# Optimization experiments

Measured on AMD Instinct MI355X. Metric: run time of the kernel, lower is better.

## Reference

```python
import jax, jax.numpy as jnp
import numpy as np

N_USERS = 100000
N_ITEMS = 50000
N_NODES = N_USERS + N_ITEMS
N_EDGES = 1500000
EMBED = 100
BATCH = 4096


def spmm(rows, cols, vals, X):
    # sparse(N,N) @ dense(N,F) via gather + segment-sum
    return jax.ops.segment_sum(vals[:, None] * X[cols], rows, num_segments=N_NODES)


def setup_inputs() -> dict:
    key = jax.random.key(0)
    ks = jax.random.split(key, 24)
    userIdx = jax.random.randint(ks[0], (BATCH,), 0, N_USERS)
    itemIdx = jax.random.randint(ks[1], (BATCH,), N_USERS, N_NODES)  # offset item ids
    rows = jax.random.randint(ks[2], (N_EDGES,), 0, N_NODES)
    cols = jax.random.randint(ks[3], (N_EDGES,), 0, N_NODES)
    vals = jax.random.uniform(ks[4], (N_EDGES,), dtype=jnp.float32) * 0.01  # D^-1/2 A D^-1/2 scale
    s = 0.1
    uEmbd = jax.random.normal(ks[5], (N_USERS, EMBED), jnp.float32) * s
    iEmbd = jax.random.normal(ks[6], (N_ITEMS, EMBED), jnp.float32) * s
    # GNN layer 1: 100 -> 80 ; layer 2: 80 -> 50 (torch Linear => W stored (in,out) here)
    w1 = jax.random.normal(ks[7], (100, 80), jnp.float32) * s
    b1 = jnp.zeros((80,), jnp.float32)
    wi1 = jax.random.normal(ks[8], (100, 80), jnp.float32) * s
    bi1 = jnp.zeros((80,), jnp.float32)
    w2 = jax.random.normal(ks[9], (80, 50), jnp.float32) * s
    b2 = jnp.zeros((50,), jnp.float32)
    wi2 = jax.random.normal(ks[10], (80, 50), jnp.float32) * s
    bi2 = jnp.zeros((50,), jnp.float32)
    t1w = jax.random.normal(ks[11], (460, 64), jnp.float32) * s
    t1b = jnp.zeros((64,), jnp.float32)
    t2w = jax.random.normal(ks[12], (64, 32), jnp.float32) * s
    t2b = jnp.zeros((32,), jnp.float32)
    t3w = jax.random.normal(ks[13], (32, 1), jnp.float32) * s
    t3b = jnp.zeros((1,), jnp.float32)
    return {"userIdx": userIdx, "itemIdx": itemIdx, "rows": rows, "cols": cols,
            "vals": vals, "uEmbd": uEmbd, "iEmbd": iEmbd,
            "w1": w1, "b1": b1, "wi1": wi1, "bi1": bi1,
            "w2": w2, "b2": b2, "wi2": wi2, "bi2": bi2,
            "t1w": t1w, "t1b": t1b, "t2w": t2w, "t2b": t2b, "t3w": t3w, "t3b": t3b}


def gnn_layer(rows, cols, vals, feats, w, b, wi, bi):
    Lx = spmm(rows, cols, vals, feats)          # L @ X
    inter = Lx * feats                          # elementwise
    part1 = (Lx + feats) @ w + b                # (L + I) @ X then linear
    part2 = spmm(rows, cols, vals, inter) @ wi + bi
    return part1 + part2


def reference(userIdx, itemIdx, rows, cols, vals, uEmbd, iEmbd,
              w1, b1, wi1, bi1, w2, b2, wi2, bi2,
              t1w, t1b, t2w, t2b, t3w, t3b):
    features = jnp.concatenate([uEmbd, iEmbd], axis=0)   # [N, 100]
    final = features
    f1 = jax.nn.relu(gnn_layer(rows, cols, vals, features, w1, b1, wi1, bi1))  # [N,80]
    final = jnp.concatenate([final, f1], axis=1)
    f2 = jax.nn.relu(gnn_layer(rows, cols, vals, f1, w2, b2, wi2, bi2))        # [N,50]
    final = jnp.concatenate([final, f2], axis=1)          # [N, 230]
    embd = jnp.concatenate([final[userIdx], final[itemIdx]], axis=1)  # [B, 460]
    embd = jax.nn.relu(embd @ t1w + t1b)
    embd = embd @ t2w + t2b
    embd = embd @ t3w + t3b
    return embd.flatten()
```

## Files before the change

kernel.cpp:

```cpp
#include <hip/hip_runtime.h>

typedef unsigned int uint;
typedef unsigned short ushort_t;
typedef __attribute__((ext_vector_type(4))) float f32x4;
typedef __attribute__((ext_vector_type(8))) short bf16x8;

#define N_USERS 100000
#define N_ITEMS 50000
#define N_NODES 150000
#define N_EDGES 1500000
#define BATCH 4096
#define NSWEEP 4
#define SWEEP_ROWS 37500

__device__ __forceinline__ uint pack_bf16x2(float a, float b) {
    uint ua = __float_as_uint(a);
    uint ub = __float_as_uint(b);
    ua = (ua + 0x7FFFu + ((ua >> 16) & 1u)) >> 16;
    ub = (ub + 0x7FFFu + ((ub >> 16) & 1u)) >> 16;
    return ua | (ub << 16);
}
__device__ __forceinline__ ushort_t cvt_bf16(float a) {
    uint ua = __float_as_uint(a);
    return (ushort_t)((ua + 0x7FFFu + ((ua >> 16) & 1u)) >> 16);
}
__device__ __forceinline__ float bf_lo(uint u) { return __uint_as_float(u << 16); }
__device__ __forceinline__ float bf_hi(uint u) { return __uint_as_float(u & 0xFFFF0000u); }

template<int P>
__device__ __forceinline__ float2 row_gather_accum(
    const int2* __restrict__ ep, int st, int d,
    const uint* __restrict__ src, int lane)
{
    float ax = 0.f, ay = 0.f;
    bool lok = lane < P;
    int2 e[12];
#pragma unroll
    for (int k = 0; k < 12; k++) e[k] = ep[st + k];
    uint b[8];
#pragma unroll
    for (int k = 0; k < 8; k++)
        b[k] = (lok && k < d) ? src[(size_t)e[k].x * P + lane] : 0u;
    for (int j = 0; j < d; j += 4) {
        uint n[4];
#pragma unroll
        for (int k = 0; k < 4; k++)
            n[k] = (lok && j + 8 + k < d) ? src[(size_t)e[8 + k].x * P + lane] : 0u;
        int2 ne[4];
#pragma unroll
        for (int k = 0; k < 4; k++) ne[k] = ep[st + j + 12 + k];
        {
            float v = __int_as_float(e[0].y);
            ax = fmaf(v, bf_lo(b[0]), ax);
            ay = fmaf(v, bf_hi(b[0]), ay);
        }
#pragma unroll
        for (int k = 1; k < 4; k++) {
            if (j + k < d) {
                float v = __int_as_float(e[k].y);
                ax = fmaf(v, bf_lo(b[k]), ax);
                ay = fmaf(v, bf_hi(b[k]), ay);
            }
        }
#pragma unroll
        for (int k = 0; k < 8; k++) e[k] = e[k + 4];
#pragma unroll
        for (int k = 0; k < 4; k++) { b[k] = b[k + 4]; b[k + 4] = n[k]; e[k + 8] = ne[k]; }
    }
    return make_float2(ax, ay);
}

__device__ __forceinline__ float2 row_gather_accum_mul(
    const int2* __restrict__ ep, int st, int d,
    const uint* __restrict__ sA, const uint* __restrict__ sB, int lane)
{
    constexpr int P = 40;
    float ax = 0.f, ay = 0.f;
    bool lok = lane < P;
    int2 e0 = ep[st],     e1 = ep[st + 1], e2 = ep[st + 2], e3 = ep[st + 3];
    int2 e4 = ep[st + 4], e5 = ep[st + 5];
    uint a0 = (lok && 0 < d) ? sA[(size_t)e0.x * P + lane] : 0u;
    uint c0 = (lok && 0 < d) ? sB[(size_t)e0.x * P + lane] : 0u;
    uint a1 = (lok && 1 < d) ? sA[(size_t)e1.x * P + lane] : 0u;
    uint c1 = (lok && 1 < d) ? sB[(size_t)e1.x * P + lane] : 0u;
    uint a2 = (lok && 2 < d) ? sA[(size_t)e2.x * P + lane] : 0u;
    uint c2 = (lok && 2 < d) ? sB[(size_t)e2.x * P + lane] : 0u;
    uint a3 = (lok && 3 < d) ? sA[(size_t)e3.x * P + lane] : 0u;
    uint c3 = (lok && 3 < d) ? sB[(size_t)e3.x * P + lane] : 0u;
    for (int j = 0; j < d; j += 2) {
        uint nA4 = (lok && j + 4 < d) ? sA[(size_t)e4.x * P + lane] : 0u;
        uint nC4 = (lok && j + 4 < d) ? sB[(size_t)e4.x * P + lane] : 0u;
        uint nA5 = (lok && j + 5 < d) ? sA[(size_t)e5.x * P + lane] : 0u;
        uint nC5 = (lok && j + 5 < d) ? sB[(size_t)e5.x * P + lane] : 0u;
        int2 n6 = ep[st + j + 6];
        int2 n7 = ep[st + j + 7];
        float v0 = __int_as_float(e0.y);
        ax = fmaf(v0, bf_lo(a0) * bf_lo(c0), ax);
        ay = fmaf(v0, bf_hi(a0) * bf_hi(c0), ay);
        if (j + 1 < d) {
            float v1 = __int_as_float(e1.y);
            ax = fmaf(v1, bf_lo(a1) * bf_lo(c1), ax);
            ay = fmaf(v1, bf_hi(a1) * bf_hi(c1), ay);
        }
        e0 = e2; a0 = a2; c0 = c2; e1 = e3; a1 = a3; c1 = c3;
        e2 = e4; a2 = nA4; c2 = nC4; e3 = e5; a3 = nA5; c3 = nC5;
        e4 = n6; e5 = n7;
    }
    return make_float2(ax, ay);
}

__global__ __launch_bounds__(256) void cast_feats(
    const float* __restrict__ uE, const float* __restrict__ iE,
    uint* __restrict__ Xb64, uint* __restrict__ Xc50)
{
    int g = blockIdx.x * 256 + threadIdx.x;
    if (g >= N_NODES * 64) return;
    int row = g >> 6, c = g & 63;
    uint outv = 0u;
    if (c < 50) {
        int e0 = c * 2;
        float a, b;
        if (row < N_USERS) { a = uE[(size_t)row * 100 + e0]; b = uE[(size_t)row * 100 + e0 + 1]; }
        else { a = iE[(size_t)(row - N_USERS) * 100 + e0]; b = iE[(size_t)(row - N_USERS) * 100 + e0 + 1]; }
        outv = pack_bf16x2(a, b);
        Xc50[(size_t)row * 50 + c] = outv;
    }
    Xb64[g] = outv;
}

__global__ __launch_bounds__(256) void prep_weights(
    const float* __restrict__ W, const float* __restrict__ Wi,
    uint* __restrict__ wtW, uint* __restrict__ wtWi)
{
    int t = blockIdx.x * 256 + threadIdx.x;
    if (t >= 2 * 80 * 64) return;
    const float* src = (t < 80 * 64) ? W : Wi;
    uint* dst = (t < 80 * 64) ? wtW : wtWi;
    int i = t % (80 * 64);
    int col = i >> 6, kk = i & 63;
    int k = kk * 2;
    uint v = 0u;
    if (k < 100) v = pack_bf16x2(src[(size_t)k * 80 + col], src[(size_t)(k + 1) * 80 + col]);
    dst[(size_t)col * 64 + kk] = v;
}

__global__ __launch_bounds__(256) void hist_kernel(
    const int* __restrict__ rows, int* __restrict__ deg, int E)
{
    int e = blockIdx.x * 256 + threadIdx.x;
    if (e < E) atomicAdd(&deg[rows[e]], 1);
}

__global__ __launch_bounds__(256) void scan_block(
    const int* __restrict__ deg, int* __restrict__ ptr,
    int* __restrict__ bsum, int n)
{
    __shared__ int s[256];
    int t = threadIdx.x;
    int i = blockIdx.x * 256 + t;
    int v = (i < n) ? deg[i] : 0;
    s[t] = v; __syncthreads();
    for (int off = 1; off < 256; off <<= 1) {
        int x = (t >= off) ? s[t - off] : 0;
        __syncthreads();
        s[t] += x;
        __syncthreads();
    }
    if (i < n) ptr[i] = s[t] - v;
    if (t == 255) bsum[blockIdx.x] = s[255];
}

__global__ __launch_bounds__(1024) void scan_tops(int* __restrict__ bsum, int nb)
{
    __shared__ int s[1024];
    int t = threadIdx.x;
    int v = (t < nb) ? bsum[t] : 0;
    s[t] = v; __syncthreads();
    for (int off = 1; off < 1024; off <<= 1) {
        int x = (t >= off) ? s[t - off] : 0;
        __syncthreads();
        s[t] += x;
        __syncthreads();
    }
    if (t < nb) bsum[t] = s[t] - v;
}

__global__ __launch_bounds__(256) void scan_apply(
    int* __restrict__ ptr, const int* __restrict__ bsum,
    int* __restrict__ pos, int n)
{
    int i = blockIdx.x * 256 + threadIdx.x;
    if (i < n) {
        int p = ptr[i] + bsum[i >> 8];
        ptr[i] = p;
        pos[i] = p;
    }
}

__global__ __launch_bounds__(256) void scatter_sweep(
    const int* __restrict__ rows, const int* __restrict__ cols,
    const float* __restrict__ vals, int* __restrict__ pos,
    int2* __restrict__ ep, int E, int lo, int hi)
{
    int e = blockIdx.x * 256 + threadIdx.x;
    if (e >= E) return;
    int r = rows[e];
    if (r < lo || r >= hi) return;
    int p = atomicAdd(&pos[r], 1);
    ep[p] = make_int2(cols[e], __float_as_int(vals[e]));
}

__global__ __launch_bounds__(256) void build_selmap(
    const int* __restrict__ userIdx, const int* __restrict__ itemIdx,
    int* __restrict__ selMap)
{
    int i = blockIdx.x * 256 + threadIdx.x;
    if (i < BATCH) selMap[userIdx[i]] = i;
    else if (i < 2 * BATCH) selMap[itemIdx[i - BATCH]] = i;
}

__global__ __launch_bounds__(256) void mark_needed(
    const int* __restrict__ userIdx, const int* __restrict__ itemIdx,
    const int* __restrict__ ptr_, const int* __restrict__ deg_,
    const int2* __restrict__ ep, int* __restrict__ flag)
{
    int i = blockIdx.x * 4 + ((int)threadIdx.x >> 6);
    if (i >= 2 * BATCH) return;
    int lane = threadIdx.x & 63;
    int row = (i < BATCH) ? userIdx[i] : itemIdx[i - BATCH];
    if (lane == 0) flag[row] = 1;
    int st = ptr_[row], d = deg_[row];
    for (int j = lane; j < d; j += 64)
        flag[ep[st + j].x] = 1;
}

__global__ __launch_bounds__(256) void compact_list(
    const int* __restrict__ flag, const int* __restrict__ fpre,
    const int* __restrict__ bsum, int* __restrict__ list,
    int* __restrict__ count, int n)
{
    int i = blockIdx.x * 256 + threadIdx.x;
    if (i < n) {
        int base = fpre[i] + bsum[i >> 8];
        if (flag[i]) list[base] = i;
        if (i == n - 1) *count = base + flag[i];
    }
}


__global__ __launch_bounds__(256) void spmm_pass1(
    const int* __restrict__ ptr_, const int* __restrict__ deg_,
    const int2* __restrict__ ep, const uint* __restrict__ Xc,
    uint* __restrict__ B1b, uint* __restrict__ INTb, int N)
{
    int row = blockIdx.x * 4 + ((int)threadIdx.x >> 6);
    if (row >= N) return;
    int lane = threadIdx.x & 63;
    float2 r = row_gather_accum<50>(ep, ptr_[row], deg_[row], Xc, lane);
    B1b[(size_t)row * 64 + lane] = pack_bf16x2(r.x, r.y);
    if (lane < 50) {
        uint xb = Xc[(size_t)row * 50 + lane];
        INTb[(size_t)row * 50 + lane] = pack_bf16x2(r.x * bf_lo(xb), r.y * bf_hi(xb));
    }
}

__global__ __launch_bounds__(256) void spmm_pass2(
    const int* __restrict__ ptr_, const int* __restrict__ deg_,
    const int2* __restrict__ ep, const uint* __restrict__ INTb,
    uint* __restrict__ B2b, int N)
{
    int row = blockIdx.x * 4 + ((int)threadIdx.x >> 6);
    if (row >= N) return;
    int lane = threadIdx.x & 63;
    float2 r = row_gather_accum<50>(ep, ptr_[row], deg_[row], INTb, lane);
    B2b[(size_t)row * 64 + lane] = pack_bf16x2(r.x, r.y);
}

__global__ __launch_bounds__(256) void spmm_pass3(
    const int* __restrict__ list, const int* __restrict__ count,
    const int* __restrict__ ptr_, const int* __restrict__ deg_,
    const int2* __restrict__ ep, const uint* __restrict__ F1b,
    const int* __restrict__ selMap,
    uint* __restrict__ Lxb, float* __restrict__ Lxsel)
{
    int idx = blockIdx.x * 4 + ((int)threadIdx.x >> 6);
    if (idx >= *count) return;
    int row = list[idx];
    int lane = threadIdx.x & 63;
    float2 r = row_gather_accum<40>(ep, ptr_[row], deg_[row], F1b, lane);
    if (lane < 40) {
        Lxb[(size_t)row * 40 + lane] = pack_bf16x2(r.x, r.y);
        int sm = selMap[row];
        if (sm >= 0)
            ((float2*)(Lxsel + (size_t)sm * 80))[lane] = r;
    }
}

__global__ __launch_bounds__(256) void spmm_pass4(
    const int* __restrict__ ptr_, const int* __restrict__ deg_,
    const int2* __restrict__ ep,
    const uint* __restrict__ Lxb, const uint* __restrict__ F1b,
    const int* __restrict__ userIdx, const int* __restrict__ itemIdx,
    float* __restrict__ outC)
{
    int i = blockIdx.x * 4 + ((int)threadIdx.x >> 6);
    if (i >= 2 * BATCH) return;
    int row = (i < BATCH) ? userIdx[i] : itemIdx[i - BATCH];
    int lane = threadIdx.x & 63;
    float2 r = row_gather_accum_mul(ep, ptr_[row], deg_[row], Lxb, F1b, lane);
    if (lane < 40)
        ((float2*)(outC + (size_t)i * 80))[lane] = r;
}

__global__ __launch_bounds__(256) void gemm1_mfma(
    const uint* __restrict__ B1b, const uint* __restrict__ Xb,
    const uint* __restrict__ B2b,
    const uint* __restrict__ wtW, const uint* __restrict__ wtWi,
    const float* __restrict__ b, const float* __restrict__ bi,
    const int* __restrict__ selMap,
    ushort_t* __restrict__ F1b, float* __restrict__ F1sel, int N)
{
    int wave = (int)threadIdx.x >> 6;
    int lane = (int)threadIdx.x & 63;
    int rowBase = blockIdx.x * 64 + wave * 16;
    int colLocal = lane & 15;
    int q = lane >> 4;
    int arow = rowBase + colLocal;
    bool rowOK = arow < N;

    f32x4 acc[5];
#pragma unroll
    for (int nt = 0; nt < 5; nt++) acc[nt] = (f32x4){0.f, 0.f, 0.f, 0.f};

    const bf16x8 zfrag = {};
    size_t aoff = (size_t)arow * 64 + q * 4;

#pragma unroll
    for (int ks = 0; ks < 4; ks++) {
        bf16x8 aL = rowOK ? *(const bf16x8*)(B1b + aoff + ks * 16) : zfrag;
        bf16x8 aX = rowOK ? *(const bf16x8*)(Xb  + aoff + ks * 16) : zfrag;
        bf16x8 aS = rowOK ? *(const bf16x8*)(B2b + aoff + ks * 16) : zfrag;
#pragma unroll
        for (int nt = 0; nt < 5; nt++) {
            size_t boff = (size_t)(nt * 16 + colLocal) * 64 + ks * 16 + q * 4;
            bf16x8 bW  = *(const bf16x8*)(wtW  + boff);
            bf16x8 bWi = *(const bf16x8*)(wtWi + boff);
            acc[nt] = __builtin_amdgcn_mfma_f32_16x16x32_bf16(aL, bW,  acc[nt], 0, 0, 0);
            acc[nt] = __builtin_amdgcn_mfma_f32_16x16x32_bf16(aX, bW,  acc[nt], 0, 0, 0);
            acc[nt] = __builtin_amdgcn_mfma_f32_16x16x32_bf16(aS, bWi, acc[nt], 0, 0, 0);
        }
    }

    int sm[4];
    bool rok[4];
#pragma unroll
    for (int reg = 0; reg < 4; reg++) {
        int row = rowBase + q * 4 + reg;
        rok[reg] = row < N;
        sm[reg] = rok[reg] ? selMap[row] : -1;
    }
#pragma unroll
    for (int nt = 0; nt < 5; nt++) {
        int col = nt * 16 + colLocal;
        float bias = b[col] + bi[col];
#pragma unroll
        for (int reg = 0; reg < 4; reg++) {
            if (!rok[reg]) continue;
            int row = rowBase + q * 4 + reg;
            float v = fmaxf(acc[nt][reg] + bias, 0.f);
            F1b[(size_t)row * 80 + col] = cvt_bf16(v);
            if (sm[reg] >= 0) F1sel[(size_t)sm[reg] * 80 + col] = v;
        }
    }
}

__global__ __launch_bounds__(256) void gemm_fused2_sel(
    const float* __restrict__ Lxsel, const float* __restrict__ F1sel,
    const int* __restrict__ selMap,
    const float* __restrict__ S2c,
    const float* __restrict__ W, const float* __restrict__ b,
    const float* __restrict__ Wi, const float* __restrict__ bi,
    const int* __restrict__ userIdx, const int* __restrict__ itemIdx,
    float* __restrict__ outC)
{
    constexpr int K = 80, M = 50, TPR = 2, MT = M / TPR;
    __shared__ float sW[K * M];
    __shared__ float sWi[K * M];
    for (int i = threadIdx.x; i < K * M; i += 256) {
        sW[i]  = W[i];
        sWi[i] = Wi[i];
    }
    __syncthreads();

    int i = blockIdx.x * (256 / TPR) + (int)threadIdx.x / TPR;
    int mBase = ((int)threadIdx.x % TPR) * MT;
    if (i >= 2 * BATCH) return;
    int r = (i < BATCH) ? userIdx[i] : itemIdx[i - BATCH];
    int sm = selMap[r];

    const float* xrow = F1sel + (size_t)sm * K;
    const float* lrow = Lxsel + (size_t)sm * K;
    const float* srow = S2c + (size_t)i * K;

    float acc[MT];
#pragma unroll
    for (int m = 0; m < MT; m++) acc[m] = 0.0f;

    for (int k4 = 0; k4 < K; k4 += 4) {
        float4 lv = *(const float4*)(lrow + k4);
        float4 xv = *(const float4*)(xrow + k4);
        float4 sv = *(const float4*)(srow + k4);
        float a[4] = {lv.x + xv.x, lv.y + xv.y, lv.z + xv.z, lv.w + xv.w};
        float s[4] = {sv.x, sv.y, sv.z, sv.w};
#pragma unroll
        for (int kk = 0; kk < 4; kk++) {
            const float* wk  = &sW[(k4 + kk) * M + mBase];
            const float* wik = &sWi[(k4 + kk) * M + mBase];
#pragma unroll
            for (int m = 0; m < MT; m++)
                acc[m] = fmaf(a[kk], wk[m], fmaf(s[kk], wik[m], acc[m]));
        }
    }

    float* orow = outC + (size_t)i * M + mBase;
#pragma unroll
    for (int m = 0; m < MT; m++)
        orow[m] = fmaxf(acc[m] + b[mBase + m] + bi[mBase + m], 0.0f);
}

template<int K, int M, int TPR, bool RELU>
__global__ __launch_bounds__(256) void mlp_gemm(
    const float* __restrict__ A,
    const float* __restrict__ W, const float* __restrict__ b,
    float* __restrict__ out, int N)
{
    __shared__ float sW[K * M];
    for (int i = threadIdx.x; i < K * M; i += 256) sW[i] = W[i];
    __syncthreads();

    constexpr int RPB = 256 / TPR;
    constexpr int MT  = M / TPR;
    int r = blockIdx.x * RPB + (int)threadIdx.x / TPR;
    int mBase = ((int)threadIdx.x % TPR) * MT;
    if (r >= N) return;

    const float* arow = A + (size_t)r * K;
    float acc[MT];
#pragma unroll
    for (int m = 0; m < MT; m++) acc[m] = 0.0f;

    for (int k = 0; k < K; k++) {
        float a = arow[k];
#pragma unroll
        for (int m = 0; m < MT; m++)
            acc[m] = fmaf(a, sW[k * M + mBase + m], acc[m]);
    }

    float* orow = out + (size_t)r * M + mBase;
#pragma unroll
    for (int m = 0; m < MT; m++) {
        float vv = acc[m] + b[mBase + m];
        orow[m] = RELU ? fmaxf(vv, 0.0f) : vv;
    }
}

__global__ __launch_bounds__(128) void gather_embd(
    const int* __restrict__ userIdx, const int* __restrict__ itemIdx,
    const float* __restrict__ uE, const float* __restrict__ iE,
    const float* __restrict__ F1sel, const int* __restrict__ selMap,
    const float* __restrict__ f2c,
    float* __restrict__ emb)
{
    int bi = blockIdx.x;
    int u  = userIdx[bi];
    int it = itemIdx[bi];
    int su = selMap[u];
    int si = selMap[it];
    float* orow = emb + (size_t)bi * 460;
    for (int c = threadIdx.x; c < 460; c += 128) {
        float val;
        if (c < 100) {
            val = (u < N_USERS) ? uE[(size_t)u * 100 + c]
                                : iE[(size_t)(u - N_USERS) * 100 + c];
        } else if (c < 180) {
            val = F1sel[(size_t)su * 80 + (c - 100)];
        } else if (c < 230) {
            val = f2c[(size_t)bi * 50 + (c - 180)];
        } else if (c < 330) {
            int cc = c - 230;
            val = (it < N_USERS) ? uE[(size_t)it * 100 + cc]
                                 : iE[(size_t)(it - N_USERS) * 100 + cc];
        } else if (c < 410) {
            val = F1sel[(size_t)si * 80 + (c - 330)];
        } else {
            val = f2c[(size_t)(BATCH + bi) * 50 + (c - 410)];
        }
        orow[c] = val;
    }
}

extern "C" void kernel_launch(void* const* d_in, const int* in_sizes, int n_in,
                              void* d_out, int out_size, void* d_ws, size_t ws_size,
                              hipStream_t stream) {
    const int*   userIdx = (const int*)d_in[0];
    const int*   itemIdx = (const int*)d_in[1];
    const int*   rows    = (const int*)d_in[2];
    const int*   cols    = (const int*)d_in[3];
    const float* vals    = (const float*)d_in[4];
    const float* uEmbd   = (const float*)d_in[5];
    const float* iEmbd   = (const float*)d_in[6];
    const float* w1      = (const float*)d_in[7];
    const float* b1      = (const float*)d_in[8];
    const float* wi1     = (const float*)d_in[9];
    const float* bi1     = (const float*)d_in[10];
    const float* w2      = (const float*)d_in[11];
    const float* b2      = (const float*)d_in[12];
    const float* wi2     = (const float*)d_in[13];
    const float* bi2     = (const float*)d_in[14];
    const float* t1w     = (const float*)d_in[15];
    const float* t1b     = (const float*)d_in[16];
    const float* t2w     = (const float*)d_in[17];
    const float* t2b     = (const float*)d_in[18];
    const float* t3w     = (const float*)d_in[19];
    const float* t3b     = (const float*)d_in[20];

    float* ws = (float*)d_ws;
    uint*  Xb64  = (uint*)ws;
    uint*  Xc50  = (uint*)(ws + 9600000);
    uint*  B1b   = (uint*)(ws + 17100000);
    uint*  Lxb   = B1b;
    uint*  INTb  = (uint*)(ws + 26700000);
    uint*  F1b   = INTb;
    uint*  B2b   = (uint*)(ws + 34200000);
    uint*  wtW   = (uint*)(ws + 43800000);
    uint*  wtWi  = (uint*)(ws + 43805120);
    float* F1sel = ws + 43810240;
    float* Lxsel = ws + 44465600;
    float* B2c   = ws + 45120960;
    float* F2c   = ws + 45776320;
    float* EMB   = ws + 46185920;
    float* H1    = ws + 48070080;
    float* H2    = ws + 48332224;
    int*   deg   = (int*)(ws + 48463296);
    int*   ptr   = deg + 150000;
    int*   pos   = ptr + 150000;
    int*   bsum  = pos + 150000;
    int2*  ep    = (int2*)(bsum + 1024);
    int*   flag  = (int*)(ep + 1500016);
    int*   fpre  = flag + 150000;
    int*   list  = fpre + 150000;
    int*   bsum2 = list + 150000;
    int*   cnt   = bsum2 + 1024;
    int*   selMap= cnt + 1;

    const int E = N_EDGES;
    dim3 blk(256);

    cast_feats<<<(N_NODES * 64 + 255) / 256, blk, 0, stream>>>(uEmbd, iEmbd, Xb64, Xc50);
    prep_weights<<<(2 * 80 * 64 + 255) / 256, blk, 0, stream>>>(w1, wi1, wtW, wtWi);

    hipMemsetAsync(deg, 0, 150000 * sizeof(int), stream);
    hipMemsetAsync(flag, 0, 150000 * sizeof(int), stream);
    hipMemsetAsync(selMap, 0xFF, 150000 * sizeof(int), stream);
    hist_kernel<<<(E + 255) / 256, blk, 0, stream>>>(rows, deg, E);
    int nScanBlocks = (N_NODES + 255) / 256;
    scan_block<<<nScanBlocks, blk, 0, stream>>>(deg, ptr, bsum, N_NODES);
    scan_tops<<<1, dim3(1024), 0, stream>>>(bsum, nScanBlocks);
    scan_apply<<<nScanBlocks, blk, 0, stream>>>(ptr, bsum, pos, N_NODES);
    for (int s = 0; s < NSWEEP; s++) {
        scatter_sweep<<<(E + 255) / 256, blk, 0, stream>>>(
            rows, cols, vals, pos, ep, E, s * SWEEP_ROWS, (s + 1) * SWEEP_ROWS);
    }

    build_selmap<<<(2 * BATCH + 255) / 256, blk, 0, stream>>>(userIdx, itemIdx, selMap);
    mark_needed<<<(2 * BATCH + 3) / 4, blk, 0, stream>>>(
        userIdx, itemIdx, ptr, deg, ep, flag);
    scan_block<<<nScanBlocks, blk, 0, stream>>>(flag, fpre, bsum2, N_NODES);
    scan_tops<<<1, dim3(1024), 0, stream>>>(bsum2, nScanBlocks);
    compact_list<<<nScanBlocks, blk, 0, stream>>>(flag, fpre, bsum2, list, cnt, N_NODES);

    int rowGrid = (N_NODES + 3) / 4;
    int selGrid = (2 * BATCH + 3) / 4;

    spmm_pass1<<<rowGrid, blk, 0, stream>>>(ptr, deg, ep, Xc50, B1b, INTb, N_NODES);
    spmm_pass2<<<rowGrid, blk, 0, stream>>>(ptr, deg, ep, INTb, B2b, N_NODES);
    {
        int grid = (N_NODES + 63) / 64;
        gemm1_mfma<<<grid, blk, 0, stream>>>(
            B1b, Xb64, B2b, wtW, wtWi, b1, bi1, selMap,
            (ushort_t*)F1b, F1sel, N_NODES);
    }

    spmm_pass3<<<rowGrid, blk, 0, stream>>>(
        list, cnt, ptr, deg, ep, F1b, selMap, Lxb, Lxsel);
    spmm_pass4<<<selGrid, blk, 0, stream>>>(
        ptr, deg, ep, Lxb, F1b, userIdx, itemIdx, B2c);
    {
        int grid = (2 * BATCH + 127) / 128;
        gemm_fused2_sel<<<grid, blk, 0, stream>>>(
            Lxsel, F1sel, selMap, B2c, w2, b2, wi2, bi2, userIdx, itemIdx, F2c);
    }

    gather_embd<<<BATCH, dim3(128), 0, stream>>>(
        userIdx, itemIdx, uEmbd, iEmbd, F1sel, selMap, F2c, EMB);
    {
        constexpr int TPR = 8;
        int grid = (BATCH + (256 / TPR) - 1) / (256 / TPR);
        mlp_gemm<460, 64, TPR, true><<<grid, blk, 0, stream>>>(
            EMB, t1w, t1b, H1, BATCH);
    }
    {
        constexpr int TPR = 4;
        int grid = (BATCH + (256 / TPR) - 1) / (256 / TPR);
        mlp_gemm<64, 32, TPR, false><<<grid, blk, 0, stream>>>(
            H1, t2w, t2b, H2, BATCH);
    }
    {
        constexpr int TPR = 1;
        int grid = (BATCH + 255) / 256;
        mlp_gemm<32, 1, TPR, false><<<grid, blk, 0, stream>>>(
            H2, t3w, t3b, (float*)d_out, BATCH);
    }
}
```

Before: 576.5 us.

## Pack four rows per wave with uint4 gathers and degree-sorted row order

The SpMM passes change from one row per 64-lane wave to four rows per wave, with 16 lanes each loading uint4 (8 bf16) chunks. Rows are bucket-sorted by degree through histogram, scan and scatter kernels so the rows sharing a wave have similar trip counts. The feature rows are padded to 52 uints for 16-byte alignment, and the edge list gets a zero tail so the loop can read past its end. This aims to cut the idle lanes (50 of 64 were used) and the underfilled waves on short rows, at the cost of extra sort kernels and rows scattered across memory.

```diff
diff --git a/kernel.cpp b/kernel.cpp
--- a/kernel.cpp
+++ b/kernel.cpp
@@ -12,6 +12,7 @@
 #define BATCH 4096
 #define NSWEEP 4
 #define SWEEP_ROWS 37500
+#define EP_PAD 96
 
 __device__ __forceinline__ uint pack_bf16x2(float a, float b) {
     uint ua = __float_as_uint(a);
@@ -27,47 +28,29 @@
 __device__ __forceinline__ float bf_lo(uint u) { return __uint_as_float(u << 16); }
 __device__ __forceinline__ float bf_hi(uint u) { return __uint_as_float(u & 0xFFFF0000u); }
 
-template<int P>
-__device__ __forceinline__ float2 row_gather_accum(
-    const int2* __restrict__ ep, int st, int d,
-    const uint* __restrict__ src, int lane)
-{
-    float ax = 0.f, ay = 0.f;
-    bool lok = lane < P;
-    int2 e[12];
-#pragma unroll
-    for (int k = 0; k < 12; k++) e[k] = ep[st + k];
-    uint b[8];
-#pragma unroll
-    for (int k = 0; k < 8; k++)
-        b[k] = (lok && k < d) ? src[(size_t)e[k].x * P + lane] : 0u;
-    for (int j = 0; j < d; j += 4) {
-        uint n[4];
-#pragma unroll
-        for (int k = 0; k < 4; k++)
-            n[k] = (lok && j + 8 + k < d) ? src[(size_t)e[8 + k].x * P + lane] : 0u;
-        int2 ne[4];
-#pragma unroll
-        for (int k = 0; k < 4; k++) ne[k] = ep[st + j + 12 + k];
-        {
-            float v = __int_as_float(e[0].y);
-            ax = fmaf(v, bf_lo(b[0]), ax);
-            ay = fmaf(v, bf_hi(b[0]), ay);
-        }
-#pragma unroll
-        for (int k = 1; k < 4; k++) {
-            if (j + k < d) {
-                float v = __int_as_float(e[k].y);
-                ax = fmaf(v, bf_lo(b[k]), ax);
-                ay = fmaf(v, bf_hi(b[k]), ay);
-            }
-        }
-#pragma unroll
-        for (int k = 0; k < 8; k++) e[k] = e[k + 4];
-#pragma unroll
-        for (int k = 0; k < 4; k++) { b[k] = b[k + 4]; b[k + 4] = n[k]; e[k + 8] = ne[k]; }
-    }
-    return make_float2(ax, ay);
+template<int PU4>
+__device__ __forceinline__ void group_gather(
+    const int2* __restrict__ ep, int st, int d, int dmax,
+    const uint* __restrict__ src, int l,
+    float aLo[4], float aHi[4])
+{
+    const uint4* s4 = (const uint4*)src;
+    bool lok = l < PU4;
+    int2 e0 = ep[st];
+    int2 e1 = ep[st + 1];
+    uint4 g0 = {0u, 0u, 0u, 0u};
+    if (lok && 0 < d) g0 = s4[(size_t)(uint)e0.x * PU4 + l];
+    for (int j = 0; j < dmax; j++) {
+        int2 e2 = ep[st + j + 2];
+        uint4 g1 = {0u, 0u, 0u, 0u};
+        if (lok && j + 1 < d) g1 = s4[(size_t)(uint)e1.x * PU4 + l];
+        float v = (j < d) ? __int_as_float(e0.y) : 0.f;
+        aLo[0] = fmaf(v, bf_lo(g0.x), aLo[0]); aHi[0] = fmaf(v, bf_hi(g0.x), aHi[0]);
+        aLo[1] = fmaf(v, bf_lo(g0.y), aLo[1]); aHi[1] = fmaf(v, bf_hi(g0.y), aHi[1]);
+        aLo[2] = fmaf(v, bf_lo(g0.z), aLo[2]); aHi[2] = fmaf(v, bf_hi(g0.z), aHi[2]);
+        aLo[3] = fmaf(v, bf_lo(g0.w), aLo[3]); aHi[3] = fmaf(v, bf_hi(g0.w), aHi[3]);
+        e0 = e1; e1 = e2; g0 = g1;
+    }
 }
 
 __device__ __forceinline__ float2 row_gather_accum_mul(
@@ -111,7 +94,7 @@
 
 __global__ __launch_bounds__(256) void cast_feats(
     const float* __restrict__ uE, const float* __restrict__ iE,
-    uint* __restrict__ Xb64, uint* __restrict__ Xc50)
+    uint* __restrict__ Xb64, uint* __restrict__ Xc52)
 {
     int g = blockIdx.x * 256 + threadIdx.x;
     if (g >= N_NODES * 64) return;
@@ -123,9 +106,9 @@
         if (row < N_USERS) { a = uE[(size_t)row * 100 + e0]; b = uE[(size_t)row * 100 + e0 + 1]; }
         else { a = iE[(size_t)(row - N_USERS) * 100 + e0]; b = iE[(size_t)(row - N_USERS) * 100 + e0 + 1]; }
         outv = pack_bf16x2(a, b);
-        Xc50[(size_t)row * 50 + c] = outv;
     }
     Xb64[g] = outv;
+    if (c < 52) Xc52[(size_t)row * 52 + c] = outv;
 }
 
 __global__ __launch_bounds__(256) void prep_weights(
@@ -210,6 +193,12 @@
     ep[p] = make_int2(cols[e], __float_as_int(vals[e]));
 }
 
+__global__ __launch_bounds__(128) void pad_ep(int2* __restrict__ ep)
+{
+    int t = threadIdx.x;
+    if (t < EP_PAD) ep[N_EDGES + t] = make_int2(0, 0);
+}
+
 __global__ __launch_bounds__(256) void build_selmap(
     const int* __restrict__ userIdx, const int* __restrict__ itemIdx,
     int* __restrict__ selMap)
@@ -234,65 +223,141 @@
         flag[ep[st + j].x] = 1;
 }
 
-__global__ __launch_bounds__(256) void compact_list(
-    const int* __restrict__ flag, const int* __restrict__ fpre,
-    const int* __restrict__ bsum, int* __restrict__ list,
-    int* __restrict__ count, int n)
+__global__ __launch_bounds__(256) void deg_hist(
+    const int* __restrict__ deg, const int* __restrict__ flag,
+    int* __restrict__ hist, int n)
 {
     int i = blockIdx.x * 256 + threadIdx.x;
-    if (i < n) {
-        int base = fpre[i] + bsum[i >> 8];
-        if (flag[i]) list[base] = i;
-        if (i == n - 1) *count = base + flag[i];
-    }
+    if (i >= n) return;
+    if (flag && !flag[i]) return;
+    int b = deg[i]; if (b > 63) b = 63;
+    atomicAdd(&hist[b], 1);
+}
+
+__global__ __launch_bounds__(64) void bins_scan(
+    const int* __restrict__ hist, int* __restrict__ pos, int* __restrict__ total)
+{
+    __shared__ int s[64];
+    int t = threadIdx.x;
+    int v = hist[t];
+    s[t] = v; __syncthreads();
+    for (int off = 1; off < 64; off <<= 1) {
+        int x = (t >= off) ? s[t - off] : 0;
+        __syncthreads();
+        s[t] += x;
+        __syncthreads();
+    }
+    pos[t] = s[t] - v;
+    if (t == 63 && total) *total = s[63];
+}
+
+__global__ __launch_bounds__(256) void deg_scatter(
+    const int* __restrict__ deg, const int* __restrict__ flag,
+    int* __restrict__ pos, int* __restrict__ sorted, int n)
+{
+    int i = blockIdx.x * 256 + threadIdx.x;
+    if (i >= n) return;
+    if (flag && !flag[i]) return;
+    int b = deg[i]; if (b > 63) b = 63;
+    int p = atomicAdd(&pos[b], 1);
+    sorted[p] = i;
 }
 
 
 __global__ __launch_bounds__(256) void spmm_pass1(
+    const int* __restrict__ sortedAll,
     const int* __restrict__ ptr_, const int* __restrict__ deg_,
     const int2* __restrict__ ep, const uint* __restrict__ Xc,
     uint* __restrict__ B1b, uint* __restrict__ INTb, int N)
 {
-    int row = blockIdx.x * 4 + ((int)threadIdx.x >> 6);
-    if (row >= N) return;
-    int lane = threadIdx.x & 63;
-    float2 r = row_gather_accum<50>(ep, ptr_[row], deg_[row], Xc, lane);
-    B1b[(size_t)row * 64 + lane] = pack_bf16x2(r.x, r.y);
-    if (lane < 50) {
-        uint xb = Xc[(size_t)row * 50 + lane];
-        INTb[(size_t)row * 50 + lane] = pack_bf16x2(r.x * bf_lo(xb), r.y * bf_hi(xb));
+    int wave = (int)threadIdx.x >> 6, lane = (int)threadIdx.x & 63;
+    int grp = lane >> 4, l = lane & 15;
+    int si = blockIdx.x * 16 + wave * 4 + grp;
+    bool valid = si < N;
+    int row = valid ? sortedAll[si] : 0;
+    int d = valid ? deg_[row] : 0;
+    int st = valid ? ptr_[row] : 0;
+    int dm = d, t;
+    t = __shfl_xor(dm, 16); dm = dm > t ? dm : t;
+    t = __shfl_xor(dm, 32); dm = dm > t ? dm : t;
+    float aLo[4] = {0.f, 0.f, 0.f, 0.f}, aHi[4] = {0.f, 0.f, 0.f, 0.f};
+    group_gather<13>(ep, st, d, dm, Xc, l, aLo, aHi);
+    if (!valid) return;
+    uint4 o = {0u, 0u, 0u, 0u};
+    if (l < 13) {
+        o.x = pack_bf16x2(aLo[0], aHi[0]); o.y = pack_bf16x2(aLo[1], aHi[1]);
+        o.z = pack_bf16x2(aLo[2], aHi[2]); o.w = pack_bf16x2(aLo[3], aHi[3]);
+    }
+    ((uint4*)(B1b + (size_t)row * 64))[l] = o;
+    if (l < 13) {
+        uint4 x = ((const uint4*)(Xc + (size_t)row * 52))[l];
+        uint4 p;
+        p.x = pack_bf16x2(aLo[0] * bf_lo(x.x), aHi[0] * bf_hi(x.x));
+        p.y = pack_bf16x2(aLo[1] * bf_lo(x.y), aHi[1] * bf_hi(x.y));
+        p.z = pack_bf16x2(aLo[2] * bf_lo(x.z), aHi[2] * bf_hi(x.z));
+        p.w = pack_bf16x2(aLo[3] * bf_lo(x.w), aHi[3] * bf_hi(x.w));
+        ((uint4*)(INTb + (size_t)row * 52))[l] = p;
     }
 }
 
 __global__ __launch_bounds__(256) void spmm_pass2(
+    const int* __restrict__ sortedAll,
     const int* __restrict__ ptr_, const int* __restrict__ deg_,
     const int2* __restrict__ ep, const uint* __restrict__ INTb,
     uint* __restrict__ B2b, int N)
 {
-    int row = blockIdx.x * 4 + ((int)threadIdx.x >> 6);
-    if (row >= N) return;
-    int lane = threadIdx.x & 63;
-    float2 r = row_gather_accum<50>(ep, ptr_[row], deg_[row], INTb, lane);
-    B2b[(size_t)row * 64 + lane] = pack_bf16x2(r.x, r.y);
+    int wave = (int)threadIdx.x >> 6, lane = (int)threadIdx.x & 63;
+    int grp = lane >> 4, l = lane & 15;
+    int si = blockIdx.x * 16 + wave * 4 + grp;
+    bool valid = si < N;
+    int row = valid ? sortedAll[si] : 0;
+    int d = valid ? deg_[row] : 0;
+    int st = valid ? ptr_[row] : 0;
+    int dm = d, t;
+    t = __shfl_xor(dm, 16); dm = dm > t ? dm : t;
+    t = __shfl_xor(dm, 32); dm = dm > t ? dm : t;
+    float aLo[4] = {0.f, 0.f, 0.f, 0.f}, aHi[4] = {0.f, 0.f, 0.f, 0.f};
+    group_gather<13>(ep, st, d, dm, INTb, l, aLo, aHi);
+    if (!valid) return;
+    uint4 o = {0u, 0u, 0u, 0u};
+    if (l < 13) {
+        o.x = pack_bf16x2(aLo[0], aHi[0]); o.y = pack_bf16x2(aLo[1], aHi[1]);
+        o.z = pack_bf16x2(aLo[2], aHi[2]); o.w = pack_bf16x2(aLo[3], aHi[3]);
+    }
+    ((uint4*)(B2b + (size_t)row * 64))[l] = o;
 }
 
 __global__ __launch_bounds__(256) void spmm_pass3(
-    const int* __restrict__ list, const int* __restrict__ count,
+    const int* __restrict__ sorted3, const int* __restrict__ cnt3,
     const int* __restrict__ ptr_, const int* __restrict__ deg_,
     const int2* __restrict__ ep, const uint* __restrict__ F1b,
     const int* __restrict__ selMap,
     uint* __restrict__ Lxb, float* __restrict__ Lxsel)
 {
-    int idx = blockIdx.x * 4 + ((int)threadIdx.x >> 6);
-    if (idx >= *count) return;
-    int row = list[idx];
-    int lane = threadIdx.x & 63;
-    float2 r = row_gather_accum<40>(ep, ptr_[row], deg_[row], F1b, lane);
-    if (lane < 40) {
-        Lxb[(size_t)row * 40 + lane] = pack_bf16x2(r.x, r.y);
-        int sm = selMap[row];
-        if (sm >= 0)
-            ((float2*)(Lxsel + (size_t)sm * 80))[lane] = r;
+    int wave = (int)threadIdx.x >> 6, lane = (int)threadIdx.x & 63;
+    int grp = lane >> 4, l = lane & 15;
+    int si = blockIdx.x * 16 + wave * 4 + grp;
+    int n3 = *cnt3;
+    bool valid = si < n3;
+    int row = valid ? sorted3[si] : 0;
+    int d = valid ? deg_[row] : 0;
+    int st = valid ? ptr_[row] : 0;
+    int dm = d, t;
+    t = __shfl_xor(dm, 16); dm = dm > t ? dm : t;
+    t = __shfl_xor(dm, 32); dm = dm > t ? dm : t;
+    float aLo[4] = {0.f, 0.f, 0.f, 0.f}, aHi[4] = {0.f, 0.f, 0.f, 0.f};
+    group_gather<10>(ep, st, d, dm, F1b, l, aLo, aHi);
+    if (!valid || l >= 10) return;
+    uint4 o;
+    o.x = pack_bf16x2(aLo[0], aHi[0]); o.y = pack_bf16x2(aLo[1], aHi[1]);
+    o.z = pack_bf16x2(aLo[2], aHi[2]); o.w = pack_bf16x2(aLo[3], aHi[3]);
+    ((uint4*)(Lxb + (size_t)row * 40))[l] = o;
+    int sm = selMap[row];
+    if (sm >= 0) {
+        float4 f0 = make_float4(aLo[0], aHi[0], aLo[1], aHi[1]);
+        float4 f1 = make_float4(aLo[2], aHi[2], aLo[3], aHi[3]);
+        ((float4*)(Lxsel + (size_t)sm * 80))[2 * l]     = f0;
+        ((float4*)(Lxsel + (size_t)sm * 80))[2 * l + 1] = f1;
     }
 }
 
@@ -526,42 +591,46 @@
 
     float* ws = (float*)d_ws;
     uint*  Xb64  = (uint*)ws;
-    uint*  Xc50  = (uint*)(ws + 9600000);
-    uint*  B1b   = (uint*)(ws + 17100000);
+    uint*  Xc52  = (uint*)(ws + 9600000);
+    uint*  B1b   = (uint*)(ws + 17400000);
     uint*  Lxb   = B1b;
-    uint*  INTb  = (uint*)(ws + 26700000);
+    uint*  INTb  = (uint*)(ws + 27000000);
     uint*  F1b   = INTb;
-    uint*  B2b   = (uint*)(ws + 34200000);
-    uint*  wtW   = (uint*)(ws + 43800000);
-    uint*  wtWi  = (uint*)(ws + 43805120);
-    float* F1sel = ws + 43810240;
-    float* Lxsel = ws + 44465600;
-    float* B2c   = ws + 45120960;
-    float* F2c   = ws + 45776320;
-    float* EMB   = ws + 46185920;
-    float* H1    = ws + 48070080;
-    float* H2    = ws + 48332224;
-    int*   deg   = (int*)(ws + 48463296);
+    uint*  B2b   = (uint*)(ws + 34800000);
+    uint*  wtW   = (uint*)(ws + 44400000);
+    uint*  wtWi  = (uint*)(ws + 44405120);
+    float* F1sel = ws + 44410240;
+    float* Lxsel = ws + 45065600;
+    float* B2c   = ws + 45720960;
+    float* F2c   = ws + 46376320;
+    float* EMB   = ws + 46785920;
+    float* H1    = ws + 48670080;
+    float* H2    = ws + 48932224;
+    int*   deg   = (int*)(ws + 49063296);
     int*   ptr   = deg + 150000;
     int*   pos   = ptr + 150000;
     int*   bsum  = pos + 150000;
     int2*  ep    = (int2*)(bsum + 1024);
-    int*   flag  = (int*)(ep + 1500016);
-    int*   fpre  = flag + 150000;
-    int*   list  = fpre + 150000;
-    int*   bsum2 = list + 150000;
-    int*   cnt   = bsum2 + 1024;
-    int*   selMap= cnt + 1;
+    int*   flag  = (int*)(ep + 1500096);
+    int*   selMap= flag + 150000;
+    int*   sortedAll = selMap + 150000;
+    int*   sorted3   = sortedAll + 150000;
+    int*   hist64    = sorted3 + 150000;
+    int*   hist64b   = hist64 + 64;
+    int*   pos64     = hist64b + 64;
+    int*   pos64b    = pos64 + 64;
+    int*   cnt3      = pos64b + 64;
 
     const int E = N_EDGES;
     dim3 blk(256);
 
-    cast_feats<<<(N_NODES * 64 + 255) / 256, blk, 0, stream>>>(uEmbd, iEmbd, Xb64, Xc50);
+    cast_feats<<<(N_NODES * 64 + 255) / 256, blk, 0, stream>>>(uEmbd, iEmbd, Xb64, Xc52);
     prep_weights<<<(2 * 80 * 64 + 255) / 256, blk, 0, stream>>>(w1, wi1, wtW, wtWi);
 
     hipMemsetAsync(deg, 0, 150000 * sizeof(int), stream);
     hipMemsetAsync(flag, 0, 150000 * sizeof(int), stream);
     hipMemsetAsync(selMap, 0xFF, 150000 * sizeof(int), stream);
+    hipMemsetAsync(hist64, 0, 128 * sizeof(int), stream);
     hist_kernel<<<(E + 255) / 256, blk, 0, stream>>>(rows, deg, E);
     int nScanBlocks = (N_NODES + 255) / 256;
     scan_block<<<nScanBlocks, blk, 0, stream>>>(deg, ptr, bsum, N_NODES);
@@ -571,19 +640,26 @@
         scatter_sweep<<<(E + 255) / 256, blk, 0, stream>>>(
             rows, cols, vals, pos, ep, E, s * SWEEP_ROWS, (s + 1) * SWEEP_ROWS);
     }
+    pad_ep<<<1, dim3(128), 0, stream>>>(ep);
 
     build_selmap<<<(2 * BATCH + 255) / 256, blk, 0, stream>>>(userIdx, itemIdx, selMap);
     mark_needed<<<(2 * BATCH + 3) / 4, blk, 0, stream>>>(
         userIdx, itemIdx, ptr, deg, ep, flag);
-    scan_block<<<nScanBlocks, blk, 0, stream>>>(flag, fpre, bsum2, N_NODES);
-    scan_tops<<<1, dim3(1024), 0, stream>>>(bsum2, nScanBlocks);
-    compact_list<<<nScanBlocks, blk, 0, stream>>>(flag, fpre, bsum2, list, cnt, N_NODES);
-
-    int rowGrid = (N_NODES + 3) / 4;
+
+    deg_hist<<<nScanBlocks, blk, 0, stream>>>(deg, nullptr, hist64, N_NODES);
+    deg_hist<<<nScanBlocks, blk, 0, stream>>>(deg, flag, hist64b, N_NODES);
+    bins_scan<<<1, dim3(64), 0, stream>>>(hist64, pos64, nullptr);
+    bins_scan<<<1, dim3(64), 0, stream>>>(hist64b, pos64b, cnt3);
+    deg_scatter<<<nScanBlocks, blk, 0, stream>>>(deg, nullptr, pos64, sortedAll, N_NODES);
+    deg_scatter<<<nScanBlocks, blk, 0, stream>>>(deg, flag, pos64b, sorted3, N_NODES);
+
+    int grpGrid = (N_NODES + 15) / 16;
     int selGrid = (2 * BATCH + 3) / 4;
 
-    spmm_pass1<<<rowGrid, blk, 0, stream>>>(ptr, deg, ep, Xc50, B1b, INTb, N_NODES);
-    spmm_pass2<<<rowGrid, blk, 0, stream>>>(ptr, deg, ep, INTb, B2b, N_NODES);
+    spmm_pass1<<<grpGrid, blk, 0, stream>>>(
+        sortedAll, ptr, deg, ep, Xc52, B1b, INTb, N_NODES);
+    spmm_pass2<<<grpGrid, blk, 0, stream>>>(
+        sortedAll, ptr, deg, ep, INTb, B2b, N_NODES);
     {
         int grid = (N_NODES + 63) / 64;
         gemm1_mfma<<<grid, blk, 0, stream>>>(
@@ -591,8 +667,8 @@
             (ushort_t*)F1b, F1sel, N_NODES);
     }
 
-    spmm_pass3<<<rowGrid, blk, 0, stream>>>(
-        list, cnt, ptr, deg, ep, F1b, selMap, Lxb, Lxsel);
+    spmm_pass3<<<grpGrid, blk, 0, stream>>>(
+        sorted3, cnt3, ptr, deg, ep, F1b, selMap, Lxb, Lxsel);
     spmm_pass4<<<selGrid, blk, 0, stream>>>(
         ptr, deg, ep, Lxb, F1b, userIdx, itemIdx, B2c);
     {
```

Result: slower. 1.951 ms (+238.4%).
